# Optimization experiments

Measured on AMD Instinct MI355X. Metric: run time of the kernel, lower is better.

The kernel has to match this reference:

```python
import jax, jax.numpy as jnp
import numpy as np

B, T, F, UNITS = 64, 512, 128, 512
EPS = 1e-3  # Keras LayerNormalization default epsilon


def _layer_norm(x, g, b):
    m = x.mean(-1, keepdims=True)
    v = x.var(-1, keepdims=True)
    return (x - m) * jax.lax.rsqrt(v + EPS) * g + b


def _lstm(x, W, U, b):
    # Keras LSTM, gate order [i, f, c, o], zero initial state, tanh activations.
    Bsz = x.shape[0]
    Un = U.shape[0]
    h0 = jnp.zeros((Bsz, Un), x.dtype)
    c0 = jnp.zeros((Bsz, Un), x.dtype)
    xW = x @ W + b  # precompute input projection: [B, T, 4U]

    def step(carry, xw_t):
        h, c = carry
        z = xw_t + h @ U
        i, f, g, o = jnp.split(z, 4, axis=-1)
        c = jax.nn.sigmoid(f) * c + jax.nn.sigmoid(i) * jnp.tanh(g)
        h = jax.nn.sigmoid(o) * jnp.tanh(c)
        return (h, c), h

    (h, c), hs = jax.lax.scan(step, (h0, c0), jnp.swapaxes(xW, 0, 1))
    return jnp.swapaxes(hs, 0, 1), h, c  # seq out [B,T,U], final h, c


def _block(x, l0, l1, Wt, bt):
    block_in = x
    # layer 0: LSTM -> LayerNorm
    W, U, b, g, be = l0
    h, _, _ = _lstm(x, W, U, b)
    out = _layer_norm(h, g, be)
    # layer 1: LSTM -> LayerNorm -> Highway (units match layer 0)
    W, U, b, g, be = l1
    h, _, _ = _lstm(out, W, U, b)
    Hx = _layer_norm(h, g, be)
    Tx = jax.nn.sigmoid(out @ Wt + bt)  # transform gate, bias init -1.5
    hw = Hx * Tx + (1.0 - Tx) * out
    # quasi-dense: concat block input with last layer output
    return jnp.concatenate([block_in, hw], axis=-1)


def setup_inputs() -> dict:
    key = jax.random.key(0)
    ks = iter(jax.random.split(key, 32))
    def nrm(shape, scale):
        return jax.random.normal(next(ks), shape, jnp.float32) * scale
    d = {"x": jax.random.normal(next(ks), (B, T, F), jnp.float32)}
    in_dims = {"00": F, "01": UNITS, "10": F + UNITS, "11": UNITS}
    for tag, ind in in_dims.items():
        d[f"W{tag}"] = nrm((ind, 4 * UNITS), 1.0 / np.sqrt(ind))
        d[f"U{tag}"] = nrm((UNITS, 4 * UNITS), 1.0 / np.sqrt(UNITS))
        d[f"b{tag}"] = jnp.zeros((4 * UNITS,), jnp.float32)
        d[f"g{tag}"] = jnp.ones((UNITS,), jnp.float32)
        d[f"be{tag}"] = jnp.zeros((UNITS,), jnp.float32)
    for blk in ("0", "1"):
        d[f"Wt{blk}"] = nrm((UNITS, UNITS), 1.0 / np.sqrt(UNITS))
        d[f"bt{blk}"] = jnp.full((UNITS,), -1.5, jnp.float32)
    return d


def reference(x,
              W00, U00, b00, g00, be00,
              W01, U01, b01, g01, be01,
              Wt0, bt0,
              W10, U10, b10, g10, be10,
              W11, U11, b11, g11, be11,
              Wt1, bt1):
    out0 = _block(x, (W00, U00, b00, g00, be00), (W01, U01, b01, g01, be01), Wt0, bt0)
    out1 = _block(out0, (W10, U10, b10, g10, be10), (W11, U11, b11, g11, be11), Wt1, bt1)
    return out1  # [B, T, F + 2*UNITS]
```

## Files before the change

### kernel.cpp

```cpp
#include <hip/hip_runtime.h>
#include <hip/hip_bf16.h>

typedef unsigned short u16;
typedef unsigned int u32;
typedef unsigned long long u64;
typedef __attribute__((ext_vector_type(8))) short short8;
typedef __attribute__((ext_vector_type(4))) short short4v;
typedef __attribute__((ext_vector_type(4))) float float4v;
typedef __attribute__((ext_vector_type(2))) float float2v;
typedef __attribute__((ext_vector_type(2))) unsigned int uint2v;
typedef __attribute__((ext_vector_type(4))) unsigned int uint4v;

#define Bsz 64
#define Tsz 512
#define Fsz 128
#define Usz 512
#define Gsz 2048
#define Msz 32768
#define OUTW 1152
#define BINW 640
#define NWG 16
#define FLSTR 32

__device__ __forceinline__ u16 f2b(float f) {
  u32 u = __float_as_uint(f);
  u32 r = (u + 0x7fffu + ((u >> 16) & 1u)) >> 16;
  return (u16)r;
}
__device__ __forceinline__ float b2f(u16 h) {
  return __uint_as_float(((u32)h) << 16);
}
__device__ __forceinline__ float sigm(float x) { return 1.f / (1.f + __expf(-x)); }
__device__ __forceinline__ float tanhfast(float x) { return 2.f / (1.f + __expf(-2.f * x)) - 1.f; }

__global__ void k_wt(const float* __restrict__ src, u16* __restrict__ dst, int K, int N,
                     const float* __restrict__ scale) {
  __shared__ float t[32][33];
  int k0 = blockIdx.y << 5, n0 = blockIdx.x << 5;
  int tid = threadIdx.x;
  int r = tid >> 3, c = (tid & 7) << 2;
  float4v v = *(const float4v*)(src + (size_t)(k0 + r) * N + n0 + c);
  float s = scale ? scale[k0 + r] : 1.f;
  t[r][c + 0] = v[0] * s; t[r][c + 1] = v[1] * s;
  t[r][c + 2] = v[2] * s; t[r][c + 3] = v[3] * s;
  __syncthreads();
  short4v o;
  o[0] = (short)f2b(t[c + 0][r]);
  o[1] = (short)f2b(t[c + 1][r]);
  o[2] = (short)f2b(t[c + 2][r]);
  o[3] = (short)f2b(t[c + 3][r]);
  *(short4v*)(dst + (size_t)(n0 + r) * K + k0 + c) = o;
}

__global__ void k_pq(const float* __restrict__ W, const float* __restrict__ g,
                     const float* __restrict__ be, const float* __restrict__ b1,
                     float* __restrict__ p, float* __restrict__ q) {
  int n = blockIdx.x * 256 + threadIdx.x;
  float sp = 0.f, sq = 0.f;
  for (int k = 0; k < Usz; ++k) {
    float w = W[(size_t)k * Gsz + n];
    sp += w * g[k]; sq += w * be[k];
  }
  p[n] = sp; q[n] = sq + b1[n];
}

__global__ void k_cvx(const float* __restrict__ x, float* __restrict__ dout, u16* __restrict__ bin) {
  int id = blockIdx.x * 256 + threadIdx.x;
  int row = id >> 5, c = (id & 31) << 2;
  float4v v = *(const float4v*)(x + (size_t)row * Fsz + c);
  *(float4v*)(dout + (size_t)row * OUTW + c) = v;
  short4v o;
  o[0] = (short)f2b(v[0]); o[1] = (short)f2b(v[1]);
  o[2] = (short)f2b(v[2]); o[3] = (short)f2b(v[3]);
  *(short4v*)(bin + (size_t)row * BINW + c) = o;
}

template <int APERM, int CPERM>
__launch_bounds__(256)
__global__ void k_gemm(const u16* __restrict__ A, int lda,
                       const u16* __restrict__ Bt, int K, int N,
                       const float* __restrict__ bias,
                       u16* __restrict__ C) {
  __shared__ u16 Al[128][40];
  __shared__ u16 Bl[64][40];
  int tid = threadIdx.x;
  int lane = tid & 63, wid = tid >> 6;
  int n0 = blockIdx.x << 6;
  size_t m0 = (size_t)blockIdx.y << 7;
  int mr = lane & 15, ko = (lane >> 4) << 3;
  float4v acc[2][4];
#pragma unroll
  for (int i = 0; i < 2; ++i)
#pragma unroll
    for (int j = 0; j < 4; ++j) acc[i][j] = (float4v){0.f, 0.f, 0.f, 0.f};

  for (int k0 = 0; k0 < K; k0 += 32) {
#pragma unroll
    for (int i = 0; i < 2; ++i) {
      int id = tid + (i << 8);
      int row = id >> 2, kc = (id & 3) << 3;
      int mlog = (int)m0 + row;
      size_t rp = APERM ? ((size_t)(mlog & 63) << 9) + (mlog >> 6) : (size_t)mlog;
      *(short8*)&Al[row][kc] = *(const short8*)(A + rp * (size_t)lda + k0 + kc);
    }
    {
      int row = tid >> 2, kc = (tid & 3) << 3;
      *(short8*)&Bl[row][kc] = *(const short8*)(Bt + (size_t)(n0 + row) * K + k0 + kc);
    }
    __syncthreads();
    short8 af0 = *(short8*)&Al[(wid << 5) + mr][ko];
    short8 af1 = *(short8*)&Al[(wid << 5) + 16 + mr][ko];
    short8 bf0 = *(short8*)&Bl[mr][ko];
    short8 bf1 = *(short8*)&Bl[16 + mr][ko];
    short8 bf2 = *(short8*)&Bl[32 + mr][ko];
    short8 bf3 = *(short8*)&Bl[48 + mr][ko];
    acc[0][0] = __builtin_amdgcn_mfma_f32_16x16x32_bf16(af0, bf0, acc[0][0], 0, 0, 0);
    acc[0][1] = __builtin_amdgcn_mfma_f32_16x16x32_bf16(af0, bf1, acc[0][1], 0, 0, 0);
    acc[0][2] = __builtin_amdgcn_mfma_f32_16x16x32_bf16(af0, bf2, acc[0][2], 0, 0, 0);
    acc[0][3] = __builtin_amdgcn_mfma_f32_16x16x32_bf16(af0, bf3, acc[0][3], 0, 0, 0);
    acc[1][0] = __builtin_amdgcn_mfma_f32_16x16x32_bf16(af1, bf0, acc[1][0], 0, 0, 0);
    acc[1][1] = __builtin_amdgcn_mfma_f32_16x16x32_bf16(af1, bf1, acc[1][1], 0, 0, 0);
    acc[1][2] = __builtin_amdgcn_mfma_f32_16x16x32_bf16(af1, bf2, acc[1][2], 0, 0, 0);
    acc[1][3] = __builtin_amdgcn_mfma_f32_16x16x32_bf16(af1, bf3, acc[1][3], 0, 0, 0);
    __syncthreads();
  }
  int rbase = (lane >> 4) << 2;
#pragma unroll
  for (int mt = 0; mt < 2; ++mt)
#pragma unroll
    for (int nt = 0; nt < 4; ++nt) {
      int n = n0 + (nt << 4) + mr;
      float bv = bias[n];
#pragma unroll
      for (int r = 0; r < 4; ++r) {
        int mlog = (int)m0 + (wid << 5) + (mt << 4) + rbase + r;
        float val = acc[mt][nt][r] + bv;
        if (CPERM) {
          int b = mlog & 63, tt = mlog >> 6;
          int u = n & 511, g = n >> 9;
          C[((((size_t)tt * 512 + u) * 64 + b) << 2) + g] = f2b(val);
        } else {
          C[(size_t)mlog * N + n] = f2b(val);
        }
      }
    }
}

__global__ void k_zero(u32* __restrict__ p, int n32) {
  int id = blockIdx.x * 256 + threadIdx.x;
  for (int i = id; i < n32; i += gridDim.x * 256) p[i] = 0u;
}

__launch_bounds__(256, 1)
__global__ void k_scan2(const u16* __restrict__ xw2,
                        const u16* __restrict__ Ut0,
                        const u16* __restrict__ Wg1,
                        const u16* __restrict__ Ut1,
                        const float* __restrict__ p1,
                        const float* __restrict__ q1,
                        const float* __restrict__ g0v,
                        const float* __restrict__ be0v,
                        u16* __restrict__ hn0,
                        u16* __restrict__ hn1,
                        u16* __restrict__ h1seq,
                        u16* __restrict__ mid,
                        u32* __restrict__ bar) {
  __shared__ u16 hl0[32768];
  __shared__ u16 hl1[32768];
  __shared__ u16 hout[2048];
  __shared__ float stats[128];
  int tid = threadIdx.x;
  int lane = tid & 63, wid = tid >> 6;
  int mr = lane & 15, cg = lane >> 4;
  int gate = mr & 3, du = mr >> 2;

  if (blockIdx.x < 16) {
    int w = blockIdx.x;
    int u0 = (w << 5) + (wid << 3);
    short8 af[2][16];
#pragma unroll
    for (int mt = 0; mt < 2; ++mt) {
      size_t urow = (size_t)(gate * Usz + u0 + (mt << 2) + du) * Usz;
#pragma unroll
      for (int kk = 0; kk < 16; ++kk)
        af[mt][kk] = *(const short8*)(Ut0 + urow + (kk << 5) + (cg << 3));
    }
    float cst[2][4];
#pragma unroll
    for (int mt = 0; mt < 2; ++mt)
#pragma unroll
      for (int nt = 0; nt < 4; ++nt) cst[mt][nt] = 0.f;

    short4v xwc[2][4], xwn[2][4];
#pragma unroll
    for (int mt = 0; mt < 2; ++mt)
#pragma unroll
      for (int nt = 0; nt < 4; ++nt)
        xwc[mt][nt] = *(const short4v*)(xw2 + ((((size_t)0 * 512 + u0 + (mt << 2) + cg) * 64
                                               + (nt << 4) + mr) << 2));

    for (int t = 0; t < Tsz; ++t) {
      float4v acc[2][4];
#pragma unroll
      for (int mt = 0; mt < 2; ++mt)
#pragma unroll
        for (int nt = 0; nt < 4; ++nt)
          acc[mt][nt] = (float4v){b2f((u16)xwc[mt][nt][0]), b2f((u16)xwc[mt][nt][1]),
                                  b2f((u16)xwc[mt][nt][2]), b2f((u16)xwc[mt][nt][3])};
      if (t + 1 < Tsz) {
#pragma unroll
        for (int mt = 0; mt < 2; ++mt)
#pragma unroll
          for (int nt = 0; nt < 4; ++nt)
            xwn[mt][nt] = *(const short4v*)(xw2 + ((((size_t)(t + 1) * 512 + u0 + (mt << 2) + cg) * 64
                                                   + (nt << 4) + mr) << 2));
      }

      if (t > 0) {
        if (wid == 0) {
          for (;;) {
            int pass = 1;
            if (lane < 16) {
              u32 v = __hip_atomic_load(bar + lane * FLSTR, __ATOMIC_RELAXED, __HIP_MEMORY_SCOPE_AGENT);
              pass = (v >= (u32)t);
            } else if (lane < 32 && t >= 4) {
              u32 v = __hip_atomic_load(bar + 2048 + (lane - 16) * FLSTR, __ATOMIC_RELAXED, __HIP_MEMORY_SCOPE_AGENT);
              pass = (v >= (u32)(t - 3));
            }
            if (__all(pass)) break;
            __builtin_amdgcn_s_sleep(1);
          }
          __threadfence();
        }
        __syncthreads();

        {
          const char* hsrc = (const char*)(hn0 + (size_t)((t - 1) & 3) * 32768);
#pragma unroll
          for (int j = 0; j < 16; ++j) {
            int c = (wid << 4) + j;
            const char* src = hsrc + ((((c & 3) << 4) + mr) << 10) + ((c >> 2) << 6) + (cg << 4);
            __builtin_amdgcn_global_load_lds(
                (const __attribute__((address_space(1))) void*)src,
                (__attribute__((address_space(3))) void*)(hl0 + (c << 9)),
                16, 0, 0);
          }
        }
        __syncthreads();

#pragma unroll
        for (int kk = 0; kk < 16; ++kk) {
          short8 bfr[4];
#pragma unroll
          for (int nt = 0; nt < 4; ++nt)
            bfr[nt] = *(const short8*)(hl0 + ((((kk << 2) + nt) << 9) + (lane << 3)));
#pragma unroll
          for (int mt = 0; mt < 2; ++mt)
#pragma unroll
            for (int nt = 0; nt < 4; ++nt)
              acc[mt][nt] = __builtin_amdgcn_mfma_f32_16x16x32_bf16(af[mt][kk], bfr[nt], acc[mt][nt], 0, 0, 0);
        }
      }

      u16 hb[2][4];
#pragma unroll
      for (int mt = 0; mt < 2; ++mt)
#pragma unroll
        for (int nt = 0; nt < 4; ++nt) {
          float zi = acc[mt][nt][0], zf = acc[mt][nt][1];
          float zg = acc[mt][nt][2], zo = acc[mt][nt][3];
          float c = sigm(zf) * cst[mt][nt] + sigm(zi) * tanhfast(zg);
          cst[mt][nt] = c;
          hb[mt][nt] = f2b(sigm(zo) * tanhfast(c));
        }

#pragma unroll
      for (int mt = 0; mt < 2; ++mt)
#pragma unroll
        for (int nt = 0; nt < 4; ++nt) {
          int b = (nt << 4) + mr;
          int ul = (wid << 3) + (mt << 2) + cg;
          *(u16*)((char*)hout + (b << 6) + ((ul << 1) ^ ((b & 7) << 3))) = hb[mt][nt];
        }
      __syncthreads();

      {
        int b = tid >> 2, q = tid & 3, s = (b & 7) << 3;
        const char* hrow = (const char*)hout + (b << 6);
        uint2v A0 = *(const uint2v*)(hrow + (((q << 4) | 0) ^ s));
        uint2v A1 = *(const uint2v*)(hrow + (((q << 4) | 8) ^ s));
        uint4v val; val[0] = A0[0]; val[1] = A0[1]; val[2] = A1[0]; val[3] = A1[1];
        *(uint4v*)((char*)(hn0 + (size_t)(t & 3) * 32768) + (b << 10) + (w << 6) + (q << 4)) = val;
      }
      __syncthreads();

      if (tid == 0)
        __hip_atomic_store(bar + w * FLSTR, (u32)(t + 1), __ATOMIC_RELEASE, __HIP_MEMORY_SCOPE_AGENT);

      if (t + 1 < Tsz) {
#pragma unroll
        for (int mt = 0; mt < 2; ++mt)
#pragma unroll
          for (int nt = 0; nt < 4; ++nt) xwc[mt][nt] = xwn[mt][nt];
      }
    }
  } else {
    int w = blockIdx.x - 16;
    int u0 = (w << 5) + (wid << 3);
    short8 afw[2][16], afu[2][16];
#pragma unroll
    for (int mt = 0; mt < 2; ++mt) {
      size_t urow = (size_t)(gate * Usz + u0 + (mt << 2) + du) * Usz;
#pragma unroll
      for (int kk = 0; kk < 16; ++kk) {
        afw[mt][kk] = *(const short8*)(Wg1 + urow + (kk << 5) + (cg << 3));
        afu[mt][kk] = *(const short8*)(Ut1 + urow + (kk << 5) + (cg << 3));
      }
    }
    float pv[2][4], qv[2][4];
#pragma unroll
    for (int mt = 0; mt < 2; ++mt)
#pragma unroll
      for (int r = 0; r < 4; ++r) {
        int n = r * 512 + u0 + (mt << 2) + cg;
        pv[mt][r] = p1[n]; qv[mt][r] = q1[n];
      }
    float gv[8], bev[8];
#pragma unroll
    for (int j = 0; j < 8; ++j) {
      gv[j] = g0v[(w << 5) + (cg << 3) + j];
      bev[j] = be0v[(w << 5) + (cg << 3) + j];
    }
    float cst[2][4];
#pragma unroll
    for (int mt = 0; mt < 2; ++mt)
#pragma unroll
      for (int nt = 0; nt < 4; ++nt) cst[mt][nt] = 0.f;

    for (int t = 0; t < Tsz; ++t) {
      if (wid == 0) {
        for (;;) {
          int pass = 1;
          if (lane < 16) {
            u32 v = __hip_atomic_load(bar + lane * FLSTR, __ATOMIC_RELAXED, __HIP_MEMORY_SCOPE_AGENT);
            pass = (v >= (u32)(t + 1));
          } else if (lane < 32 && t > 0) {
            u32 v = __hip_atomic_load(bar + 2048 + (lane - 16) * FLSTR, __ATOMIC_RELAXED, __HIP_MEMORY_SCOPE_AGENT);
            pass = (v >= (u32)t);
          }
          if (__all(pass)) break;
          __builtin_amdgcn_s_sleep(1);
        }
        __threadfence();
      }
      __syncthreads();

      {
        const char* hsrc = (const char*)(hn0 + (size_t)(t & 3) * 32768);
#pragma unroll
        for (int j = 0; j < 16; ++j) {
          int c = (wid << 4) + j;
          const char* src = hsrc + ((((c & 3) << 4) + mr) << 10) + ((c >> 2) << 6) + (cg << 4);
          __builtin_amdgcn_global_load_lds(
              (const __attribute__((address_space(1))) void*)src,
              (__attribute__((address_space(3))) void*)(hl0 + (c << 9)),
              16, 0, 0);
        }
      }
      if (t > 0) {
        const char* hsrc = (const char*)(hn1 + (size_t)((t - 1) & 1) * 32768);
#pragma unroll
        for (int j = 0; j < 16; ++j) {
          int c = (wid << 4) + j;
          const char* src = hsrc + ((((c & 3) << 4) + mr) << 10) + ((c >> 2) << 6) + (cg << 4);
          __builtin_amdgcn_global_load_lds(
              (const __attribute__((address_space(1))) void*)src,
              (__attribute__((address_space(3))) void*)(hl1 + (c << 9)),
              16, 0, 0);
        }
      }
      __syncthreads();

      {
        float s = 0.f, sq = 0.f;
#pragma unroll
        for (int kk = 0; kk < 16; ++kk) {
          short8 hv = *(const short8*)(hl0 + ((((kk << 2) + wid) << 9) + (lane << 3)));
#pragma unroll
          for (int j = 0; j < 8; ++j) { float x = b2f((u16)hv[j]); s += x; sq += x * x; }
        }
        s += __shfl_xor(s, 16); s += __shfl_xor(s, 32);
        sq += __shfl_xor(sq, 16); sq += __shfl_xor(sq, 32);
        float m = s * (1.f / 512.f);
        float var = sq * (1.f / 512.f) - m * m;
        float rs = rsqrtf(var + 1e-3f);
        if (lane < 16) { stats[((wid << 4) + lane) * 2] = m; stats[((wid << 4) + lane) * 2 + 1] = rs; }
      }

      float4v aW[2][4], aU[2][4];
#pragma unroll
      for (int mt = 0; mt < 2; ++mt)
#pragma unroll
        for (int nt = 0; nt < 4; ++nt) { aW[mt][nt] = (float4v){0.f,0.f,0.f,0.f}; aU[mt][nt] = (float4v){0.f,0.f,0.f,0.f}; }
#pragma unroll
      for (int kk = 0; kk < 16; ++kk) {
        short8 bfr[4];
#pragma unroll
        for (int nt = 0; nt < 4; ++nt)
          bfr[nt] = *(const short8*)(hl0 + ((((kk << 2) + nt) << 9) + (lane << 3)));
#pragma unroll
        for (int mt = 0; mt < 2; ++mt)
#pragma unroll
          for (int nt = 0; nt < 4; ++nt)
            aW[mt][nt] = __builtin_amdgcn_mfma_f32_16x16x32_bf16(afw[mt][kk], bfr[nt], aW[mt][nt], 0, 0, 0);
      }
      if (t > 0) {
#pragma unroll
        for (int kk = 0; kk < 16; ++kk) {
          short8 bfr[4];
#pragma unroll
          for (int nt = 0; nt < 4; ++nt)
            bfr[nt] = *(const short8*)(hl1 + ((((kk << 2) + nt) << 9) + (lane << 3)));
#pragma unroll
          for (int mt = 0; mt < 2; ++mt)
#pragma unroll
            for (int nt = 0; nt < 4; ++nt)
              aU[mt][nt] = __builtin_amdgcn_mfma_f32_16x16x32_bf16(afu[mt][kk], bfr[nt], aU[mt][nt], 0, 0, 0);
        }
      }
      __syncthreads();

      float2v mrs[4];
#pragma unroll
      for (int nt = 0; nt < 4; ++nt)
        mrs[nt] = *(const float2v*)&stats[((nt << 4) + mr) * 2];

      u16 hb[2][4];
#pragma unroll
      for (int mt = 0; mt < 2; ++mt)
#pragma unroll
        for (int nt = 0; nt < 4; ++nt) {
          float m = mrs[nt][0], rs = mrs[nt][1];
          float z0 = rs * (aW[mt][nt][0] - m * pv[mt][0]) + qv[mt][0] + aU[mt][nt][0];
          float z1 = rs * (aW[mt][nt][1] - m * pv[mt][1]) + qv[mt][1] + aU[mt][nt][1];
          float z2 = rs * (aW[mt][nt][2] - m * pv[mt][2]) + qv[mt][2] + aU[mt][nt][2];
          float z3 = rs * (aW[mt][nt][3] - m * pv[mt][3]) + qv[mt][3] + aU[mt][nt][3];
          float c = sigm(z1) * cst[mt][nt] + sigm(z0) * tanhfast(z2);
          cst[mt][nt] = c;
          hb[mt][nt] = f2b(sigm(z3) * tanhfast(c));
        }

#pragma unroll
      for (int mt = 0; mt < 2; ++mt)
#pragma unroll
        for (int nt = 0; nt < 4; ++nt) {
          int b = (nt << 4) + mr;
          int ul = (wid << 3) + (mt << 2) + cg;
          *(u16*)((char*)hout + (b << 6) + ((ul << 1) ^ ((b & 7) << 3))) = hb[mt][nt];
        }
      __syncthreads();

      uint4v val;
      {
        int b = tid >> 2, q = tid & 3, s = (b & 7) << 3;
        const char* hrow = (const char*)hout + (b << 6);
        uint2v A0 = *(const uint2v*)(hrow + (((q << 4) | 0) ^ s));
        uint2v A1 = *(const uint2v*)(hrow + (((q << 4) | 8) ^ s));
        val[0] = A0[0]; val[1] = A0[1]; val[2] = A1[0]; val[3] = A1[1];
        *(uint4v*)((char*)(hn1 + (size_t)(t & 1) * 32768) + (b << 10) + (w << 6) + (q << 4)) = val;
      }
      __syncthreads();

      if (tid == 0)
        __hip_atomic_store(bar + 2048 + w * FLSTR, (u32)(t + 1), __ATOMIC_RELEASE, __HIP_MEMORY_SCOPE_AGENT);

      {
        int b = tid >> 2, q = tid & 3;
        *(uint4v*)((char*)h1seq + ((size_t)t << 16) + (b << 10) + (w << 6) + (q << 4)) = val;
      }
#pragma unroll
      for (int nt = 0; nt < 4; ++nt) {
        short8 hv = *(const short8*)(hl0 + ((((w << 2) + nt) << 9) + (lane << 3)));
        float m = mrs[nt][0], rs = mrs[nt][1];
        short8 o8;
#pragma unroll
        for (int j = 0; j < 8; ++j)
          o8[j] = (short)f2b((b2f((u16)hv[j]) - m) * rs * gv[j] + bev[j]);
        int b = (nt << 4) + mr;
        *(short8*)(mid + ((size_t)t * 64 + b) * Usz + (w << 5) + (cg << 3)) = o8;
      }
    }
  }
}

__launch_bounds__(256)
__global__ void k_lnhw(const u16* __restrict__ hs, const float* __restrict__ g,
                       const float* __restrict__ be, const u16* __restrict__ txr,
                       const u16* __restrict__ ob, float* __restrict__ dout,
                       int dcol, u16* __restrict__ bin) {
  int lane = threadIdx.x & 63, wid = threadIdx.x >> 6;
  size_t row = (size_t)blockIdx.x * 4 + wid;
  short8 v = *(const short8*)(hs + row * Usz + (lane << 3));
  float f[8];
  float s = 0.f, q = 0.f;
#pragma unroll
  for (int j = 0; j < 8; ++j) { f[j] = b2f((u16)v[j]); s += f[j]; q += f[j] * f[j]; }
#pragma unroll
  for (int o = 32; o > 0; o >>= 1) { s += __shfl_xor(s, o); q += __shfl_xor(q, o); }
  float mean = s * (1.f / 512.f);
  float var = q * (1.f / 512.f) - mean * mean;
  float rs = rsqrtf(var + 1e-3f);
  float4v g0 = *(const float4v*)(g + (lane << 3));
  float4v g1 = *(const float4v*)(g + (lane << 3) + 4);
  float4v e0 = *(const float4v*)(be + (lane << 3));
  float4v e1 = *(const float4v*)(be + (lane << 3) + 4);
  short8 tv = *(const short8*)(txr + row * Usz + (lane << 3));
  short8 ov = *(const short8*)(ob + row * Usz + (lane << 3));
  float hwv[8];
#pragma unroll
  for (int j = 0; j < 8; ++j) {
    float gg = (j < 4) ? g0[j] : g1[j - 4];
    float ee = (j < 4) ? e0[j] : e1[j - 4];
    float hx = (f[j] - mean) * rs * gg + ee;
    float tx = sigm(b2f((u16)tv[j]));
    float o_ = b2f((u16)ov[j]);
    hwv[j] = hx * tx + (1.f - tx) * o_;
  }
  size_t orow = ((row & 63) << 9) + (row >> 6);
  float4v w0 = {hwv[0], hwv[1], hwv[2], hwv[3]};
  float4v w1 = {hwv[4], hwv[5], hwv[6], hwv[7]};
  *(float4v*)(dout + orow * OUTW + dcol + (lane << 3)) = w0;
  *(float4v*)(dout + orow * OUTW + dcol + (lane << 3) + 4) = w1;
  if (bin) {
    short8 hb;
#pragma unroll
    for (int j = 0; j < 8; ++j) hb[j] = (short)f2b(hwv[j]);
    *(short8*)(bin + orow * BINW + 128 + (lane << 3)) = hb;
  }
}

extern "C" void kernel_launch(void* const* d_in, const int* in_sizes, int n_in,
                              void* d_out, int out_size, void* d_ws, size_t ws_size,
                              hipStream_t stream) {
  (void)in_sizes; (void)n_in; (void)out_size; (void)ws_size;
  const float* x = (const float*)d_in[0];
  const float* W[4]  = {(const float*)d_in[1],  (const float*)d_in[6],
                        (const float*)d_in[11], (const float*)d_in[16]};
  const float* U[4]  = {(const float*)d_in[2],  (const float*)d_in[7],
                        (const float*)d_in[12], (const float*)d_in[17]};
  const float* bb_[4] = {(const float*)d_in[3],  (const float*)d_in[8],
                        (const float*)d_in[13], (const float*)d_in[18]};
  const float* gg_[4] = {(const float*)d_in[4],  (const float*)d_in[9],
                        (const float*)d_in[14], (const float*)d_in[19]};
  const float* be_[4] = {(const float*)d_in[5],  (const float*)d_in[10],
                        (const float*)d_in[15], (const float*)d_in[20]};
  const float* Wtr[2] = {(const float*)d_in[21], (const float*)d_in[23]};
  const float* btr[2] = {(const float*)d_in[22], (const float*)d_in[24]};

  char* ws = (char*)d_ws;
  size_t off = 0;
  u16* xwb   = (u16*)(ws + off); off += (size_t)Msz * Gsz * 2;
  u16* h1seq = (u16*)(ws + off); off += (size_t)Msz * Usz * 2;
  u16* mid   = (u16*)(ws + off); off += (size_t)Msz * Usz * 2;
  u16* bin   = (u16*)(ws + off); off += (size_t)Msz * BINW * 2;
  const int KIN[4] = {128, 512, 640, 512};
  u16* Wtb[4];
  for (int i = 0; i < 4; ++i) { Wtb[i] = (u16*)(ws + off); off += (size_t)Gsz * KIN[i] * 2; }
  u16* Utb[4];
  for (int i = 0; i < 4; ++i) { Utb[i] = (u16*)(ws + off); off += (size_t)Gsz * Usz * 2; }
  u16* Wtrb[2];
  for (int i = 0; i < 2; ++i) { Wtrb[i] = (u16*)(ws + off); off += (size_t)Usz * Usz * 2; }
  float* pq = (float*)(ws + off); off += 4 * Gsz * 4;
  u16* hn0 = (u16*)(ws + off); off += 4 * (size_t)Bsz * Usz * 2;
  u16* hn1 = (u16*)(ws + off); off += 2 * (size_t)Bsz * Usz * 2;
  u32* bar = (u32*)(ws + off); off += 16384;
  float* dout = (float*)d_out;

  k_wt<<<dim3(Gsz / 32, KIN[0] / 32), 256, 0, stream>>>(W[0], Wtb[0], KIN[0], Gsz, nullptr);
  k_wt<<<dim3(Gsz / 32, KIN[1] / 32), 256, 0, stream>>>(W[1], Wtb[1], KIN[1], Gsz, gg_[0]);
  k_wt<<<dim3(Gsz / 32, KIN[2] / 32), 256, 0, stream>>>(W[2], Wtb[2], KIN[2], Gsz, nullptr);
  k_wt<<<dim3(Gsz / 32, KIN[3] / 32), 256, 0, stream>>>(W[3], Wtb[3], KIN[3], Gsz, gg_[2]);
  for (int i = 0; i < 4; ++i)
    k_wt<<<dim3(Gsz / 32, Usz / 32), 256, 0, stream>>>(U[i], Utb[i], Usz, Gsz, nullptr);
  for (int i = 0; i < 2; ++i)
    k_wt<<<dim3(Usz / 32, Usz / 32), 256, 0, stream>>>(Wtr[i], Wtrb[i], Usz, Usz, nullptr);
  k_pq<<<8, 256, 0, stream>>>(W[1], gg_[0], be_[0], bb_[1], pq + 0 * Gsz, pq + 1 * Gsz);
  k_pq<<<8, 256, 0, stream>>>(W[3], gg_[2], be_[2], bb_[3], pq + 2 * Gsz, pq + 3 * Gsz);

  k_cvx<<<(Msz * 32) / 256, 256, 0, stream>>>(x, dout, bin);

  for (int blk = 0; blk < 2; ++blk) {
    int l0 = blk * 2, l1 = blk * 2 + 1;
    k_gemm<1, 1><<<dim3(Gsz / 64, Msz / 128), 256, 0, stream>>>(bin, BINW, Wtb[l0], KIN[l0], Gsz, bb_[l0], xwb);
    k_zero<<<1, 256, 0, stream>>>(bar, 4096);
    k_scan2<<<32, 256, 0, stream>>>(xwb, Utb[l0], Wtb[l1], Utb[l1],
                                    pq + (blk * 2 + 0) * Gsz, pq + (blk * 2 + 1) * Gsz,
                                    gg_[l0], be_[l0], hn0, hn1, h1seq, mid, bar);
    k_gemm<0, 0><<<dim3(Usz / 64, Msz / 128), 256, 0, stream>>>(mid, Usz, Wtrb[blk], Usz, Usz, btr[blk], xwb);
    k_lnhw<<<Msz / 4, 256, 0, stream>>>(h1seq, gg_[l1], be_[l1], xwb, mid, dout,
                                        blk == 0 ? 128 : 640, blk == 0 ? bin : (u16*)nullptr);
  }
}
```

Baseline: 12.02 ms.

## Double scan workgroup size to 8 waves, halving per-wave recurrent tile

The persistent LSTM scan kernel now launches 512 threads per workgroup instead of 256. Each wave handles 4 hidden units instead of 8, so the MFMA work, weight registers and cell state per wave are halved. The LDS staging, h write-out and LayerNorm/mid output loops are redistributed across the 8 waves, with stats and mid computed only by the first 4 waves. This aims to cut serial per-timestep latency through more wave parallelism on the critical recurrence path, at the cost of more waves taking part in barriers and smaller per-wave stores.

After: 12.77 ms. 1.06x slower.

```diff
diff --git a/kernel.cpp b/kernel.cpp
--- a/kernel.cpp
+++ b/kernel.cpp
@@ -3,7 +3,6 @@
 
 typedef unsigned short u16;
 typedef unsigned int u32;
-typedef unsigned long long u64;
 typedef __attribute__((ext_vector_type(8))) short short8;
 typedef __attribute__((ext_vector_type(4))) short short4v;
 typedef __attribute__((ext_vector_type(4))) float float4v;
@@ -151,7 +150,7 @@
   for (int i = id; i < n32; i += gridDim.x * 256) p[i] = 0u;
 }
 
-__launch_bounds__(256, 1)
+__launch_bounds__(512, 1)
 __global__ void k_scan2(const u16* __restrict__ xw2,
                         const u16* __restrict__ Ut0,
                         const u16* __restrict__ Wg1,
@@ -176,44 +175,35 @@
 
   if (blockIdx.x < 16) {
     int w = blockIdx.x;
-    int u0 = (w << 5) + (wid << 3);
-    short8 af[2][16];
-#pragma unroll
-    for (int mt = 0; mt < 2; ++mt) {
-      size_t urow = (size_t)(gate * Usz + u0 + (mt << 2) + du) * Usz;
+    int u0 = (w << 5) + (wid << 2);
+    short8 af[16];
+    {
+      size_t urow = (size_t)(gate * Usz + u0 + du) * Usz;
 #pragma unroll
       for (int kk = 0; kk < 16; ++kk)
-        af[mt][kk] = *(const short8*)(Ut0 + urow + (kk << 5) + (cg << 3));
-    }
-    float cst[2][4];
-#pragma unroll
-    for (int mt = 0; mt < 2; ++mt)
-#pragma unroll
-      for (int nt = 0; nt < 4; ++nt) cst[mt][nt] = 0.f;
-
-    short4v xwc[2][4], xwn[2][4];
-#pragma unroll
-    for (int mt = 0; mt < 2; ++mt)
+        af[kk] = *(const short8*)(Ut0 + urow + (kk << 5) + (cg << 3));
+    }
+    float cst[4];
+#pragma unroll
+    for (int nt = 0; nt < 4; ++nt) cst[nt] = 0.f;
+
+    short4v xwc[4], xwn[4];
+#pragma unroll
+    for (int nt = 0; nt < 4; ++nt)
+      xwc[nt] = *(const short4v*)(xw2 + ((((size_t)0 * 512 + u0 + cg) * 64
+                                         + (nt << 4) + mr) << 2));
+
+    for (int t = 0; t < Tsz; ++t) {
+      float4v acc[4];
 #pragma unroll
       for (int nt = 0; nt < 4; ++nt)
-        xwc[mt][nt] = *(const short4v*)(xw2 + ((((size_t)0 * 512 + u0 + (mt << 2) + cg) * 64
-                                               + (nt << 4) + mr) << 2));
-
-    for (int t = 0; t < Tsz; ++t) {
-      float4v acc[2][4];
-#pragma unroll
-      for (int mt = 0; mt < 2; ++mt)
+        acc[nt] = (float4v){b2f((u16)xwc[nt][0]), b2f((u16)xwc[nt][1]),
+                            b2f((u16)xwc[nt][2]), b2f((u16)xwc[nt][3])};
+      if (t + 1 < Tsz) {
 #pragma unroll
         for (int nt = 0; nt < 4; ++nt)
-          acc[mt][nt] = (float4v){b2f((u16)xwc[mt][nt][0]), b2f((u16)xwc[mt][nt][1]),
-                                  b2f((u16)xwc[mt][nt][2]), b2f((u16)xwc[mt][nt][3])};
-      if (t + 1 < Tsz) {
-#pragma unroll
-        for (int mt = 0; mt < 2; ++mt)
-#pragma unroll
-          for (int nt = 0; nt < 4; ++nt)
-            xwn[mt][nt] = *(const short4v*)(xw2 + ((((size_t)(t + 1) * 512 + u0 + (mt << 2) + cg) * 64
-                                                   + (nt << 4) + mr) << 2));
+          xwn[nt] = *(const short4v*)(xw2 + ((((size_t)(t + 1) * 512 + u0 + cg) * 64
+                                             + (nt << 4) + mr) << 2));
       }
 
       if (t > 0) {
@@ -237,8 +227,8 @@
         {
           const char* hsrc = (const char*)(hn0 + (size_t)((t - 1) & 3) * 32768);
 #pragma unroll
-          for (int j = 0; j < 16; ++j) {
-            int c = (wid << 4) + j;
+          for (int j = 0; j < 8; ++j) {
+            int c = (wid << 3) + j;
             const char* src = hsrc + ((((c & 3) << 4) + mr) << 10) + ((c >> 2) << 6) + (cg << 4);
             __builtin_amdgcn_global_load_lds(
                 (const __attribute__((address_space(1))) void*)src,
@@ -255,42 +245,33 @@
           for (int nt = 0; nt < 4; ++nt)
             bfr[nt] = *(const short8*)(hl0 + ((((kk << 2) + nt) << 9) + (lane << 3)));
 #pragma unroll
-          for (int mt = 0; mt < 2; ++mt)
-#pragma unroll
-            for (int nt = 0; nt < 4; ++nt)
-              acc[mt][nt] = __builtin_amdgcn_mfma_f32_16x16x32_bf16(af[mt][kk], bfr[nt], acc[mt][nt], 0, 0, 0);
-        }
-      }
-
-      u16 hb[2][4];
-#pragma unroll
-      for (int mt = 0; mt < 2; ++mt)
-#pragma unroll
-        for (int nt = 0; nt < 4; ++nt) {
-          float zi = acc[mt][nt][0], zf = acc[mt][nt][1];
-          float zg = acc[mt][nt][2], zo = acc[mt][nt][3];
-          float c = sigm(zf) * cst[mt][nt] + sigm(zi) * tanhfast(zg);
-          cst[mt][nt] = c;
-          hb[mt][nt] = f2b(sigm(zo) * tanhfast(c));
-        }
-
-#pragma unroll
-      for (int mt = 0; mt < 2; ++mt)
-#pragma unroll
-        for (int nt = 0; nt < 4; ++nt) {
-          int b = (nt << 4) + mr;
-          int ul = (wid << 3) + (mt << 2) + cg;
-          *(u16*)((char*)hout + (b << 6) + ((ul << 1) ^ ((b & 7) << 3))) = hb[mt][nt];
-        }
+          for (int nt = 0; nt < 4; ++nt)
+            acc[nt] = __builtin_amdgcn_mfma_f32_16x16x32_bf16(af[kk], bfr[nt], acc[nt], 0, 0, 0);
+        }
+      }
+
+      u16 hb[4];
+#pragma unroll
+      for (int nt = 0; nt < 4; ++nt) {
+        float zi = acc[nt][0], zf = acc[nt][1];
+        float zg = acc[nt][2], zo = acc[nt][3];
+        float c = sigm(zf) * cst[nt] + sigm(zi) * tanhfast(zg);
+        cst[nt] = c;
+        hb[nt] = f2b(sigm(zo) * tanhfast(c));
+      }
+
+#pragma unroll
+      for (int nt = 0; nt < 4; ++nt) {
+        int b = (nt << 4) + mr;
+        int ul = (wid << 2) + cg;
+        *(u16*)((char*)hout + (b << 6) + ((ul << 1) ^ ((b & 7) << 3))) = hb[nt];
+      }
       __syncthreads();
 
       {
-        int b = tid >> 2, q = tid & 3, s = (b & 7) << 3;
-        const char* hrow = (const char*)hout + (b << 6);
-        uint2v A0 = *(const uint2v*)(hrow + (((q << 4) | 0) ^ s));
-        uint2v A1 = *(const uint2v*)(hrow + (((q << 4) | 8) ^ s));
-        uint4v val; val[0] = A0[0]; val[1] = A0[1]; val[2] = A1[0]; val[3] = A1[1];
-        *(uint4v*)((char*)(hn0 + (size_t)(t & 3) * 32768) + (b << 10) + (w << 6) + (q << 4)) = val;
+        int b = tid >> 3, q = tid & 7;
+        uint2v v2 = *(const uint2v*)((char*)hout + (b << 6) + ((q ^ (b & 7)) << 3));
+        *(uint2v*)((char*)(hn0 + (size_t)(t & 3) * 32768) + (b << 10) + (w << 6) + (q << 3)) = v2;
       }
       __syncthreads();
 
@@ -299,43 +280,36 @@
 
       if (t + 1 < Tsz) {
 #pragma unroll
-        for (int mt = 0; mt < 2; ++mt)
-#pragma unroll
-          for (int nt = 0; nt < 4; ++nt) xwc[mt][nt] = xwn[mt][nt];
+        for (int nt = 0; nt < 4; ++nt) xwc[nt] = xwn[nt];
       }
     }
   } else {
     int w = blockIdx.x - 16;
-    int u0 = (w << 5) + (wid << 3);
-    short8 afw[2][16], afu[2][16];
-#pragma unroll
-    for (int mt = 0; mt < 2; ++mt) {
-      size_t urow = (size_t)(gate * Usz + u0 + (mt << 2) + du) * Usz;
+    int u0 = (w << 5) + (wid << 2);
+    short8 afw[16], afu[16];
+    {
+      size_t urow = (size_t)(gate * Usz + u0 + du) * Usz;
 #pragma unroll
       for (int kk = 0; kk < 16; ++kk) {
-        afw[mt][kk] = *(const short8*)(Wg1 + urow + (kk << 5) + (cg << 3));
-        afu[mt][kk] = *(const short8*)(Ut1 + urow + (kk << 5) + (cg << 3));
-      }
-    }
-    float pv[2][4], qv[2][4];
-#pragma unroll
-    for (int mt = 0; mt < 2; ++mt)
-#pragma unroll
-      for (int r = 0; r < 4; ++r) {
-        int n = r * 512 + u0 + (mt << 2) + cg;
-        pv[mt][r] = p1[n]; qv[mt][r] = q1[n];
-      }
+        afw[kk] = *(const short8*)(Wg1 + urow + (kk << 5) + (cg << 3));
+        afu[kk] = *(const short8*)(Ut1 + urow + (kk << 5) + (cg << 3));
+      }
+    }
+    float pv[4], qv[4];
+#pragma unroll
+    for (int r = 0; r < 4; ++r) {
+      int n = r * 512 + u0 + cg;
+      pv[r] = p1[n]; qv[r] = q1[n];
+    }
     float gv[8], bev[8];
 #pragma unroll
     for (int j = 0; j < 8; ++j) {
       gv[j] = g0v[(w << 5) + (cg << 3) + j];
       bev[j] = be0v[(w << 5) + (cg << 3) + j];
     }
-    float cst[2][4];
-#pragma unroll
-    for (int mt = 0; mt < 2; ++mt)
-#pragma unroll
-      for (int nt = 0; nt < 4; ++nt) cst[mt][nt] = 0.f;
+    float cst[4];
+#pragma unroll
+    for (int nt = 0; nt < 4; ++nt) cst[nt] = 0.f;
 
     for (int t = 0; t < Tsz; ++t) {
       if (wid == 0) {
@@ -358,8 +332,8 @@
       {
         const char* hsrc = (const char*)(hn0 + (size_t)(t & 3) * 32768);
 #pragma unroll
-        for (int j = 0; j < 16; ++j) {
-          int c = (wid << 4) + j;
+        for (int j = 0; j < 8; ++j) {
+          int c = (wid << 3) + j;
           const char* src = hsrc + ((((c & 3) << 4) + mr) << 10) + ((c >> 2) << 6) + (cg << 4);
           __builtin_amdgcn_global_load_lds(
               (const __attribute__((address_space(1))) void*)src,
@@ -370,8 +344,8 @@
       if (t > 0) {
         const char* hsrc = (const char*)(hn1 + (size_t)((t - 1) & 1) * 32768);
 #pragma unroll
-        for (int j = 0; j < 16; ++j) {
-          int c = (wid << 4) + j;
+        for (int j = 0; j < 8; ++j) {
+          int c = (wid << 3) + j;
           const char* src = hsrc + ((((c & 3) << 4) + mr) << 10) + ((c >> 2) << 6) + (cg << 4);
           __builtin_amdgcn_global_load_lds(
               (const __attribute__((address_space(1))) void*)src,
@@ -381,7 +355,7 @@
       }
       __syncthreads();
 
-      {
+      if (wid < 4) {
         float s = 0.f, sq = 0.f;
 #pragma unroll
         for (int kk = 0; kk < 16; ++kk) {
@@ -397,11 +371,9 @@
         if (lane < 16) { stats[((wid << 4) + lane) * 2] = m; stats[((wid << 4) + lane) * 2 + 1] = rs; }
       }
 
-      float4v aW[2][4], aU[2][4];
-#pragma unroll
-      for (int mt = 0; mt < 2; ++mt)
-#pragma unroll
-        for (int nt = 0; nt < 4; ++nt) { aW[mt][nt] = (float4v){0.f,0.f,0.f,0.f}; aU[mt][nt] = (float4v){0.f,0.f,0.f,0.f}; }
+      float4v aW[4], aU[4];
+#pragma unroll
+      for (int nt = 0; nt < 4; ++nt) { aW[nt] = (float4v){0.f,0.f,0.f,0.f}; aU[nt] = (float4v){0.f,0.f,0.f,0.f}; }
 #pragma unroll
       for (int kk = 0; kk < 16; ++kk) {
         short8 bfr[4];
@@ -409,10 +381,8 @@
         for (int nt = 0; nt < 4; ++nt)
           bfr[nt] = *(const short8*)(hl0 + ((((kk << 2) + nt) << 9) + (lane << 3)));
 #pragma unroll
-        for (int mt = 0; mt < 2; ++mt)
-#pragma unroll
-          for (int nt = 0; nt < 4; ++nt)
-            aW[mt][nt] = __builtin_amdgcn_mfma_f32_16x16x32_bf16(afw[mt][kk], bfr[nt], aW[mt][nt], 0, 0, 0);
+        for (int nt = 0; nt < 4; ++nt)
+          aW[nt] = __builtin_amdgcn_mfma_f32_16x16x32_bf16(afw[kk], bfr[nt], aW[nt], 0, 0, 0);
       }
       if (t > 0) {
 #pragma unroll
@@ -422,10 +392,8 @@
           for (int nt = 0; nt < 4; ++nt)
             bfr[nt] = *(const short8*)(hl1 + ((((kk << 2) + nt) << 9) + (lane << 3)));
 #pragma unroll
-          for (int mt = 0; mt < 2; ++mt)
-#pragma unroll
-            for (int nt = 0; nt < 4; ++nt)
-              aU[mt][nt] = __builtin_amdgcn_mfma_f32_16x16x32_bf16(afu[mt][kk], bfr[nt], aU[mt][nt], 0, 0, 0);
+          for (int nt = 0; nt < 4; ++nt)
+            aU[nt] = __builtin_amdgcn_mfma_f32_16x16x32_bf16(afu[kk], bfr[nt], aU[nt], 0, 0, 0);
         }
       }
       __syncthreads();
@@ -435,39 +403,32 @@
       for (int nt = 0; nt < 4; ++nt)
         mrs[nt] = *(const float2v*)&stats[((nt << 4) + mr) * 2];
 
-      u16 hb[2][4];
-#pragma unroll
-      for (int mt = 0; mt < 2; ++mt)
-#pragma unroll
-        for (int nt = 0; nt < 4; ++nt) {
-          float m = mrs[nt][0], rs = mrs[nt][1];
-          float z0 = rs * (aW[mt][nt][0] - m * pv[mt][0]) + qv[mt][0] + aU[mt][nt][0];
-          float z1 = rs * (aW[mt][nt][1] - m * pv[mt][1]) + qv[mt][1] + aU[mt][nt][1];
-          float z2 = rs * (aW[mt][nt][2] - m * pv[mt][2]) + qv[mt][2] + aU[mt][nt][2];
-          float z3 = rs * (aW[mt][nt][3] - m * pv[mt][3]) + qv[mt][3] + aU[mt][nt][3];
-          float c = sigm(z1) * cst[mt][nt] + sigm(z0) * tanhfast(z2);
-          cst[mt][nt] = c;
-          hb[mt][nt] = f2b(sigm(z3) * tanhfast(c));
-        }
-
-#pragma unroll
-      for (int mt = 0; mt < 2; ++mt)
-#pragma unroll
-        for (int nt = 0; nt < 4; ++nt) {
-          int b = (nt << 4) + mr;
-          int ul = (wid << 3) + (mt << 2) + cg;
-          *(u16*)((char*)hout + (b << 6) + ((ul << 1) ^ ((b & 7) << 3))) = hb[mt][nt];
-        }
-      __syncthreads();
-
-      uint4v val;
+      u16 hb[4];
+#pragma unroll
+      for (int nt = 0; nt < 4; ++nt) {
+        float m = mrs[nt][0], rs = mrs[nt][1];
+        float z0 = rs * (aW[nt][0] - m * pv[0]) + qv[0] + aU[nt][0];
+        float z1 = rs * (aW[nt][1] - m * pv[1]) + qv[1] + aU[nt][1];
+        float z2 = rs * (aW[nt][2] - m * pv[2]) + qv[2] + aU[nt][2];
+        float z3 = rs * (aW[nt][3] - m * pv[3]) + qv[3] + aU[nt][3];
+        float c = sigm(z1) * cst[nt] + sigm(z0) * tanhfast(z2);
+        cst[nt] = c;
+        hb[nt] = f2b(sigm(z3) * tanhfast(c));
+      }
+
+#pragma unroll
+      for (int nt = 0; nt < 4; ++nt) {
+        int b = (nt << 4) + mr;
+        int ul = (wid << 2) + cg;
+        *(u16*)((char*)hout + (b << 6) + ((ul << 1) ^ ((b & 7) << 3))) = hb[nt];
+      }
+      __syncthreads();
+
+      uint2v v2;
       {
-        int b = tid >> 2, q = tid & 3, s = (b & 7) << 3;
-        const char* hrow = (const char*)hout + (b << 6);
-        uint2v A0 = *(const uint2v*)(hrow + (((q << 4) | 0) ^ s));
-        uint2v A1 = *(const uint2v*)(hrow + (((q << 4) | 8) ^ s));
-        val[0] = A0[0]; val[1] = A0[1]; val[2] = A1[0]; val[3] = A1[1];
-        *(uint4v*)((char*)(hn1 + (size_t)(t & 1) * 32768) + (b << 10) + (w << 6) + (q << 4)) = val;
+        int b = tid >> 3, q = tid & 7;
+        v2 = *(const uint2v*)((char*)hout + (b << 6) + ((q ^ (b & 7)) << 3));
+        *(uint2v*)((char*)(hn1 + (size_t)(t & 1) * 32768) + (b << 10) + (w << 6) + (q << 3)) = v2;
       }
       __syncthreads();
 
@@ -475,18 +436,18 @@
         __hip_atomic_store(bar + 2048 + w * FLSTR, (u32)(t + 1), __ATOMIC_RELEASE, __HIP_MEMORY_SCOPE_AGENT);
 
       {
-        int b = tid >> 2, q = tid & 3;
-        *(uint4v*)((char*)h1seq + ((size_t)t << 16) + (b << 10) + (w << 6) + (q << 4)) = val;
-      }
-#pragma unroll
-      for (int nt = 0; nt < 4; ++nt) {
-        short8 hv = *(const short8*)(hl0 + ((((w << 2) + nt) << 9) + (lane << 3)));
-        float m = mrs[nt][0], rs = mrs[nt][1];
+        int b = tid >> 3, q = tid & 7;
+        *(uint2v*)((char*)h1seq + ((size_t)t << 16) + (b << 10) + (w << 6) + (q << 3)) = v2;
+      }
+      if (wid < 4) {
+        int c = (w << 2) + wid;
+        short8 hv = *(const short8*)(hl0 + ((c << 9) + (lane << 3)));
+        int b = (wid << 4) + mr;
+        float m = stats[b * 2], rs = stats[b * 2 + 1];
         short8 o8;
 #pragma unroll
         for (int j = 0; j < 8; ++j)
           o8[j] = (short)f2b((b2f((u16)hv[j]) - m) * rs * gv[j] + bev[j]);
-        int b = (nt << 4) + mr;
         *(short8*)(mid + ((size_t)t * 64 + b) * Usz + (w << 5) + (cg << 3)) = o8;
       }
     }
@@ -593,7 +554,7 @@
     int l0 = blk * 2, l1 = blk * 2 + 1;
     k_gemm<1, 1><<<dim3(Gsz / 64, Msz / 128), 256, 0, stream>>>(bin, BINW, Wtb[l0], KIN[l0], Gsz, bb_[l0], xwb);
     k_zero<<<1, 256, 0, stream>>>(bar, 4096);
-    k_scan2<<<32, 256, 0, stream>>>(xwb, Utb[l0], Wtb[l1], Utb[l1],
+    k_scan2<<<32, 512, 0, stream>>>(xwb, Utb[l0], Wtb[l1], Utb[l1],
                                     pq + (blk * 2 + 0) * Gsz, pq + (blk * 2 + 1) * Gsz,
                                     gg_[l0], be_[l0], hn0, hn1, h1seq, mid, bar);
     k_gemm<0, 0><<<dim3(Usz / 64, Msz / 128), 256, 0, stream>>>(mid, Usz, Wtrb[blk], Usz, Usz, btr[blk], xwb);
```
